# Kernel tuning notes

Hardware: AMD Instinct MI355X
Metric: run time of the kernel (lower is better)

## Reference

```python
import jax, jax.numpy as jnp
import numpy as np

N_NODES = 100000
N_EDGES = 1600000
IN_F, HID_F, N_CLS = 512, 128, 64


def spmm(row, col, val, x, n):
    # out[i] = sum_{e: row[e]==i} val[e] * x[col[e]]  (sparse adj @ x)
    msgs = val[:, None] * x[col]          # [E, F] gather + scale
    return jax.ops.segment_sum(msgs, row, num_segments=n)


def setup_inputs() -> dict:
    key = jax.random.key(0)
    k = jax.random.split(key, 8)
    x = jax.random.normal(k[0], (N_NODES, IN_F), dtype=jnp.float32)
    adj_row = jax.random.randint(k[1], (N_EDGES,), 0, N_NODES, dtype=jnp.int32)
    adj_col = jax.random.randint(k[2], (N_EDGES,), 0, N_NODES, dtype=jnp.int32)
    adj_val = jax.random.uniform(k[3], (N_EDGES,), dtype=jnp.float32)
    s1 = 1.0 / np.sqrt(IN_F)
    s2 = 1.0 / np.sqrt(HID_F)
    w1 = jax.random.uniform(k[4], (IN_F, HID_F), jnp.float32, -s1, s1)
    b1 = jax.random.uniform(k[5], (HID_F,), jnp.float32, -s1, s1)
    w2 = jax.random.uniform(k[6], (HID_F, N_CLS), jnp.float32, -s2, s2)
    b2 = jax.random.uniform(k[7], (N_CLS,), jnp.float32, -s2, s2)
    return {"x": x, "adj_row": adj_row, "adj_col": adj_col, "adj_val": adj_val,
            "w1": w1, "b1": b1, "w2": w2, "b2": b2}


def reference(x, adj_row, adj_col, adj_val, w1, b1, w2, b2):
    n = x.shape[0]
    # conv1: dense projection then sparse aggregation
    h = spmm(adj_row, adj_col, adj_val, x @ w1 + b1, n)
    h = jax.nn.relu(h)  # dropout is identity in eval mode
    # conv2
    out = spmm(adj_row, adj_col, adj_val, h @ w2 + b2, n)
    return out
```

## Files before the change

kernel.cpp:

```cpp
#include <hip/hip_runtime.h>
#include <hip/hip_bf16.h>


constexpr int N_NODES = 100000;
constexpr int IN_F    = 512;
constexpr int HID_F   = 128;
constexpr int N_CLS   = 64;
constexpr int N_EDGES = 1600000;

constexpr int SCAN_BLOCK    = 256;
constexpr int N_SCAN_BLOCKS = (N_NODES + SCAN_BLOCK - 1) / SCAN_BLOCK;
constexpr int NB_GEMM2      = (N_NODES + 255) / 256;

constexpr int NB_G1 = (N_NODES + 63) / 64;
constexpr int NB_SC = (N_EDGES + 1023) / 1024;
constexpr int NB_FUSED = NB_G1 + NB_SC;

typedef __attribute__((ext_vector_type(8))) short short8;
typedef __attribute__((ext_vector_type(4))) float f32x4;

static __device__ __forceinline__ unsigned short f2bf(float x) {
    unsigned int u = __float_as_uint(x);
    unsigned int r = (u + 0x7FFFu + ((u >> 16) & 1u)) >> 16;
    return (unsigned short)r;
}
static __device__ __forceinline__ float bf2f(unsigned short u) {
    return __uint_as_float(((unsigned int)u) << 16);
}

__global__ __launch_bounds__(256) void prep_kernel(
    const float* __restrict__ w1, const float* __restrict__ w2,
    const int* __restrict__ row,
    unsigned short* __restrict__ w1t, unsigned short* __restrict__ w2t,
    int* __restrict__ counts)
{
    const int bid = blockIdx.x;
    if (bid < 256) {
        int idx = bid * 256 + threadIdx.x;
        int n = idx >> 9, k = idx & 511;
        w1t[idx] = f2bf(w1[k * HID_F + n]);
    } else if (bid < 288) {
        int idx = (bid - 256) * 256 + threadIdx.x;
        int n = idx >> 7, k = idx & 127;
        w2t[idx] = f2bf(w2[k * N_CLS + n]);
    } else {
        int e = (bid - 288) * 256 + threadIdx.x;
        if (e < N_EDGES) atomicAdd(&counts[row[e]], 1);
    }
}

__global__ __launch_bounds__(SCAN_BLOCK) void scanA_kernel(
    const int* __restrict__ counts, int* __restrict__ local_ex,
    int* __restrict__ blockSums)
{
    __shared__ int s[SCAN_BLOCK];
    const int t = threadIdx.x;
    const int i = blockIdx.x * SCAN_BLOCK + t;
    int v = (i < N_NODES) ? counts[i] : 0;
    s[t] = v;
    __syncthreads();
    for (int off = 1; off < SCAN_BLOCK; off <<= 1) {
        int u = (t >= off) ? s[t - off] : 0;
        __syncthreads();
        s[t] += u;
        __syncthreads();
    }
    if (i < N_NODES) local_ex[i] = s[t] - v;
    if (t == SCAN_BLOCK - 1) blockSums[blockIdx.x] = s[t];
}

__global__ __launch_bounds__(512) void scanB_kernel(int* __restrict__ blockSums)
{
    __shared__ int s[512];
    const int t = threadIdx.x;
    int v = (t < N_SCAN_BLOCKS) ? blockSums[t] : 0;
    s[t] = v;
    __syncthreads();
    for (int off = 1; off < 512; off <<= 1) {
        int u = (t >= off) ? s[t - off] : 0;
        __syncthreads();
        s[t] += u;
        __syncthreads();
    }
    if (t < N_SCAN_BLOCKS) blockSums[t] = s[t] - v;
}

__global__ __launch_bounds__(SCAN_BLOCK) void scanC_kernel(
    const int* __restrict__ local_ex, const int* __restrict__ blockSums,
    int* __restrict__ row_ptr, int* __restrict__ cursor)
{
    const int i = blockIdx.x * SCAN_BLOCK + threadIdx.x;
    if (i < N_NODES) {
        int v = local_ex[i] + blockSums[blockIdx.x];
        row_ptr[i] = v;
        cursor[i]  = v;
    }
    if (i == 0) row_ptr[N_NODES] = N_EDGES;
}

__global__ __launch_bounds__(256, 4) void fused_g1_scatter_kernel(
    const float* __restrict__ x, const unsigned short* __restrict__ w1t,
    const float* __restrict__ b1, unsigned short* __restrict__ h0b,
    const int* __restrict__ row, const int* __restrict__ col,
    const float* __restrict__ val, int* __restrict__ cursor,
    int2* __restrict__ es)
{
    __shared__ unsigned short Bs[128 * 128];
    char* lb = (char*)Bs;
    const int tid = threadIdx.x;
    const int bid = blockIdx.x;

    if (bid & 1) {
        const int base = (bid >> 1) * 1024 + tid;
#pragma unroll
        for (int i = 0; i < 4; ++i) {
            int e = base + i * 256;
            if (e < N_EDGES) {
                int r = row[e];
                int pos = atomicAdd(&cursor[r], 1);
                es[pos] = make_int2(col[e], __float_as_int(val[e]));
            }
        }
        return;
    }

    const int gid  = bid >> 1;
    const int lane = tid & 63;
    const int w    = tid >> 6;
    const int m = lane & 15;
    const int q = lane >> 4;
    const int row0 = gid * 64;
    const int myrow = row0 + w * 16 + m;
    const int arow  = (myrow < N_NODES) ? myrow : (N_NODES - 1);

    f32x4 acc[8];
#pragma unroll
    for (int ni = 0; ni < 8; ++ni)
        acc[ni] = (f32x4){0.f, 0.f, 0.f, 0.f};

    union U8 { short8 v; __hip_bfloat162 h[4]; };

    const float* ap = x + (size_t)arow * IN_F + q * 8;
    const int swz = (m & 7) << 4;

    float4 a0l = ((const float4*)ap)[0];
    float4 a0h = ((const float4*)ap)[1];
    float4 a1l = ((const float4*)(ap + 32))[0];
    float4 a1h = ((const float4*)(ap + 32))[1];

#pragma unroll
    for (int t = 0; t < 16; ++t) {
        if ((t & 3) == 0) {
            if (t) __syncthreads();
            const unsigned short* src = w1t + (t >> 2) * 128;
#pragma unroll
            for (int i = 0; i < 8; ++i) {
                int c = tid + i * 256;
                int n = c >> 4, k16 = c & 15;
                short8 v = *(const short8*)(src + (size_t)n * IN_F + k16 * 8);
                *(short8*)(lb + ((n * 256 + k16 * 16) ^ ((n & 7) << 4))) = v;
            }
            __syncthreads();
        }

        float4 nl, nh;
        if (t + 2 < 16) {
            nl = ((const float4*)(ap + (t + 2) * 32))[0];
            nh = ((const float4*)(ap + (t + 2) * 32))[1];
        }

        U8 u;
        u.h[0] = __float22bfloat162_rn(make_float2(a0l.x, a0l.y));
        u.h[1] = __float22bfloat162_rn(make_float2(a0l.z, a0l.w));
        u.h[2] = __float22bfloat162_rn(make_float2(a0h.x, a0h.y));
        u.h[3] = __float22bfloat162_rn(make_float2(a0h.z, a0h.w));
        short8 av = u.v;

        const int kb = (t & 3) * 64 + q * 16;
#pragma unroll
        for (int ni = 0; ni < 8; ++ni) {
            int off = (((ni * 16 + m) << 8) + kb) ^ swz;
            short8 bfr = *(const short8*)(lb + off);
            acc[ni] = __builtin_amdgcn_mfma_f32_16x16x32_bf16(av, bfr, acc[ni], 0, 0, 0);
        }

        a0l = a1l; a0h = a1h; a1l = nl; a1h = nh;
    }

    __syncthreads();
    {
        float bias[8];
#pragma unroll
        for (int ni = 0; ni < 8; ++ni) bias[ni] = b1[ni * 16 + m];

        char* cb = lb + w * 4352;
#pragma unroll
        for (int ni = 0; ni < 8; ++ni)
#pragma unroll
            for (int r = 0; r < 4; ++r)
                *(unsigned short*)(cb + (q * 4 + r) * 272 + (ni * 16 + m) * 2) =
                    f2bf(acc[ni][r] + bias[ni]);
    }
    __syncthreads();
#pragma unroll
    for (int i = 0; i < 4; ++i) {
        int c = tid + i * 256;
        int lr = c >> 4, c16 = c & 15;
        int grow = row0 + lr;
        if (grow < N_NODES) {
            short8 v = *(const short8*)(lb + (lr >> 4) * 4352 + (lr & 15) * 272 + c16 * 16);
            *(short8*)(h0b + (size_t)grow * HID_F + c16 * 8) = v;
        }
    }
}

__global__ __launch_bounds__(512, 4) void gemm2_mfma_kernel(
    const unsigned short* __restrict__ h1r, const unsigned short* __restrict__ w2t,
    const float* __restrict__ b2, float* __restrict__ h2)
{
    __shared__ unsigned short Bs[64 * 128];
    char* lb = (char*)Bs;

    const int tid  = threadIdx.x;
    const int lane = tid & 63;
    const int w    = tid >> 6;
    const int m = lane & 15;
    const int q = lane >> 4;
    const int row0 = blockIdx.x * 256 + w * 32;
    const bool active = row0 < N_NODES;

#pragma unroll
    for (int i = 0; i < 2; ++i) {
        int chunk = tid + i * 512;
        int n   = chunk >> 4;
        int k16 = chunk & 15;
        short8 v = *(const short8*)(w2t + (size_t)n * HID_F + k16 * 8);
        *(short8*)(lb + ((n * 256 + k16 * 16) ^ ((n & 7) << 4))) = v;
    }
    __syncthreads();
    if (!active) return;

    const unsigned short* a0p = h1r + (size_t)(row0 + m)      * HID_F + q * 8;
    const unsigned short* a1p = h1r + (size_t)(row0 + 16 + m) * HID_F + q * 8;

    short8 a0[4], a1[4];
#pragma unroll
    for (int t = 0; t < 4; ++t) {
        a0[t] = *(const short8*)(a0p + t * 32);
        a1[t] = *(const short8*)(a1p + t * 32);
    }

    f32x4 acc[2][4];
#pragma unroll
    for (int mi = 0; mi < 2; ++mi)
#pragma unroll
        for (int ni = 0; ni < 4; ++ni)
            acc[mi][ni] = (f32x4){0.f, 0.f, 0.f, 0.f};

    const int swz = (m & 7) << 4;
#pragma unroll
    for (int t = 0; t < 4; ++t) {
        const int kb = t * 64 + q * 16;
#pragma unroll
        for (int ni = 0; ni < 4; ++ni) {
            int off = (((ni * 16 + m) << 8) + kb) ^ swz;
            short8 b = *(const short8*)(lb + off);
            acc[0][ni] = __builtin_amdgcn_mfma_f32_16x16x32_bf16(a0[t], b, acc[0][ni], 0, 0, 0);
            acc[1][ni] = __builtin_amdgcn_mfma_f32_16x16x32_bf16(a1[t], b, acc[1][ni], 0, 0, 0);
        }
    }

    float bias[4];
#pragma unroll
    for (int ni = 0; ni < 4; ++ni) bias[ni] = b2[ni * 16 + m];

#pragma unroll
    for (int mi = 0; mi < 2; ++mi)
#pragma unroll
        for (int r = 0; r < 4; ++r) {
            int row = row0 + mi * 16 + q * 4 + r;
            float* dst = h2 + (size_t)row * N_CLS;
#pragma unroll
            for (int ni = 0; ni < 4; ++ni)
                dst[ni * 16 + m] = acc[mi][ni][r] + bias[ni];
        }
}

__global__ __launch_bounds__(256) void spmm_g128_kernel(
    const int* __restrict__ rp, const int2* __restrict__ es,
    const unsigned short* __restrict__ src, unsigned short* __restrict__ dst)
{
    const int r = blockIdx.x * 4 + threadIdx.y;
    if (r >= N_NODES) return;
    const int lane = threadIdx.x;
    const int j0 = rp[r], j1 = rp[r + 1];

    float ax = 0.f, ay = 0.f;
    int j = j0;
    for (; j + 7 < j1; j += 8) {
        int2 e[8];
        ushort2 u[8];
#pragma unroll
        for (int t = 0; t < 8; ++t) e[t] = es[j + t];
#pragma unroll
        for (int t = 0; t < 8; ++t)
            u[t] = ((const ushort2*)(src + (size_t)e[t].x * HID_F))[lane];
#pragma unroll
        for (int t = 0; t < 8; ++t) {
            float v = __int_as_float(e[t].y);
            ax += v * bf2f(u[t].x);
            ay += v * bf2f(u[t].y);
        }
    }
    if (j + 3 < j1) {
        int2 e[4];
        ushort2 u[4];
#pragma unroll
        for (int t = 0; t < 4; ++t) e[t] = es[j + t];
#pragma unroll
        for (int t = 0; t < 4; ++t)
            u[t] = ((const ushort2*)(src + (size_t)e[t].x * HID_F))[lane];
#pragma unroll
        for (int t = 0; t < 4; ++t) {
            float v = __int_as_float(e[t].y);
            ax += v * bf2f(u[t].x);
            ay += v * bf2f(u[t].y);
        }
        j += 4;
    }
    for (; j < j1; ++j) {
        int2 e = es[j];
        float v = __int_as_float(e.y);
        ushort2 u = ((const ushort2*)(src + (size_t)e.x * HID_F))[lane];
        ax += v * bf2f(u.x);
        ay += v * bf2f(u.y);
    }
    ushort2 o;
    o.x = f2bf(fmaxf(ax, 0.f));
    o.y = f2bf(fmaxf(ay, 0.f));
    ((ushort2*)(dst + (size_t)r * HID_F))[lane] = o;
}

__global__ __launch_bounds__(256) void spmm_g64_kernel(
    const int* __restrict__ rp, const int2* __restrict__ es,
    const float* __restrict__ src, float* __restrict__ dst)
{
    const int r = blockIdx.x * 4 + threadIdx.y;
    if (r >= N_NODES) return;
    const int lane = threadIdx.x;
    const int j0 = rp[r], j1 = rp[r + 1];

    float acc = 0.f;
    int j = j0;
    for (; j + 7 < j1; j += 8) {
        int2 e[8];
        float a[8];
#pragma unroll
        for (int t = 0; t < 8; ++t) e[t] = es[j + t];
#pragma unroll
        for (int t = 0; t < 8; ++t)
            a[t] = src[(size_t)e[t].x * N_CLS + lane];
#pragma unroll
        for (int t = 0; t < 8; ++t)
            acc += __int_as_float(e[t].y) * a[t];
    }
    if (j + 3 < j1) {
        int2 e[4];
        float a[4];
#pragma unroll
        for (int t = 0; t < 4; ++t) e[t] = es[j + t];
#pragma unroll
        for (int t = 0; t < 4; ++t)
            a[t] = src[(size_t)e[t].x * N_CLS + lane];
#pragma unroll
        for (int t = 0; t < 4; ++t)
            acc += __int_as_float(e[t].y) * a[t];
        j += 4;
    }
    for (; j < j1; ++j) {
        int2 e = es[j];
        acc += __int_as_float(e.y) * src[(size_t)e.x * N_CLS + lane];
    }
    dst[(size_t)r * N_CLS + lane] = acc;
}

extern "C" void kernel_launch(void* const* d_in, const int* in_sizes, int n_in,
                              void* d_out, int out_size, void* d_ws, size_t ws_size,
                              hipStream_t stream)
{
    const float* x       = (const float*)d_in[0];
    const int*   adj_row = (const int*)  d_in[1];
    const int*   adj_col = (const int*)  d_in[2];
    const float* adj_val = (const float*)d_in[3];
    const float* w1      = (const float*)d_in[4];
    const float* b1      = (const float*)d_in[5];
    const float* w2      = (const float*)d_in[6];
    const float* b2      = (const float*)d_in[7];
    float*       out     = (float*)d_out;

    char* ws = (char*)d_ws;
    unsigned short* h0b   = (unsigned short*)ws;
    unsigned short* h1r   = (unsigned short*)(ws + 25600000);
    float*          h2    = (float*)(ws + 51200000);
    int2*           es    = (int2*) (ws + 76800000);
    int*            rp    = (int*)  (ws + 89600000);
    int*            cur   = (int*)  (ws + 90000016);
    unsigned short* w1t   = (unsigned short*)(ws + 90400016);
    int*            lex   = (int*)  (ws + 90531088);
    int*            bsum  = (int*)  (ws + 90931088);
    unsigned short* w2t   = (unsigned short*)(ws + 90932656);

    hipMemsetAsync(cur, 0, N_NODES * sizeof(int), stream);
    prep_kernel<<<288 + (N_EDGES + 255) / 256, 256, 0, stream>>>(
        w1, w2, adj_row, w1t, w2t, cur);
    scanA_kernel<<<N_SCAN_BLOCKS, SCAN_BLOCK, 0, stream>>>(cur, lex, bsum);
    scanB_kernel<<<1, 512, 0, stream>>>(bsum);
    scanC_kernel<<<N_SCAN_BLOCKS, SCAN_BLOCK, 0, stream>>>(lex, bsum, rp, cur);

    fused_g1_scatter_kernel<<<NB_FUSED, 256, 0, stream>>>(
        x, w1t, b1, h0b, adj_row, adj_col, adj_val, cur, es);
    spmm_g128_kernel<<<(N_NODES + 3) / 4, dim3(64, 4), 0, stream>>>(
        rp, es, h0b, h1r);

    gemm2_mfma_kernel<<<NB_GEMM2, 512, 0, stream>>>(h1r, w2t, b2, h2);
    spmm_g64_kernel<<<(N_NODES + 3) / 4, dim3(64, 4), 0, stream>>>(
        rp, es, h2, out);
}
```

Measured before the change: 563.2 us.

## Fuse first SpMM into GEMM2 via LDS and gather 4 edges per wave

Measured after the change: 659.5 us. 1.17x slower.

```diff
diff --git a/kernel.cpp b/kernel.cpp
--- a/kernel.cpp
+++ b/kernel.cpp
@@ -10,11 +10,11 @@
 
 constexpr int SCAN_BLOCK    = 256;
 constexpr int N_SCAN_BLOCKS = (N_NODES + SCAN_BLOCK - 1) / SCAN_BLOCK;
-constexpr int NB_GEMM2      = (N_NODES + 255) / 256;
 
 constexpr int NB_G1 = (N_NODES + 63) / 64;
 constexpr int NB_SC = (N_EDGES + 1023) / 1024;
 constexpr int NB_FUSED = NB_G1 + NB_SC;
+constexpr int NB_S1G2  = (N_NODES + 127) / 128;
 
 typedef __attribute__((ext_vector_type(8))) short short8;
 typedef __attribute__((ext_vector_type(4))) float f32x4;
@@ -214,59 +214,106 @@
     }
 }
 
-__global__ __launch_bounds__(512, 4) void gemm2_mfma_kernel(
-    const unsigned short* __restrict__ h1r, const unsigned short* __restrict__ w2t,
-    const float* __restrict__ b2, float* __restrict__ h2)
-{
-    __shared__ unsigned short Bs[64 * 128];
-    char* lb = (char*)Bs;
+__global__ __launch_bounds__(256, 3) void spmm1_gemm2_kernel(
+    const int* __restrict__ rp, const int2* __restrict__ es,
+    const unsigned short* __restrict__ h0b,
+    const unsigned short* __restrict__ w2t, const float* __restrict__ b2,
+    float* __restrict__ h2)
+{
+    __shared__ unsigned short H1[128 * 128];
+    __shared__ unsigned short W2[64 * 128];
+    char* lh = (char*)H1;
+    char* lw = (char*)W2;
 
     const int tid  = threadIdx.x;
     const int lane = tid & 63;
     const int w    = tid >> 6;
+    const int g    = lane >> 4;
+    const int l    = lane & 15;
+    const int row0 = blockIdx.x * 128;
+
+#pragma unroll
+    for (int i = 0; i < 4; ++i) {
+        int chunk = tid + i * 256;
+        int n = chunk >> 4, k16 = chunk & 15;
+        short8 v = *(const short8*)(w2t + (size_t)n * HID_F + k16 * 8);
+        *(short8*)(lw + ((n * 256 + k16 * 16) ^ ((n & 7) << 4))) = v;
+    }
+
+    for (int rr = 0; rr < 32; ++rr) {
+        const int r = row0 + w * 32 + rr;
+        if (r < N_NODES) {
+            const int j0 = rp[r], j1 = rp[r + 1];
+            float acc[8] = {0.f, 0.f, 0.f, 0.f, 0.f, 0.f, 0.f, 0.f};
+            int j = j0;
+            if (j < j1) {
+                int jj = j + g;
+                int ci = jj < j1 ? jj : j1 - 1;
+                int2 ec = es[ci];
+                float vc = jj < j1 ? __int_as_float(ec.y) : 0.f;
+                for (; j < j1; j += 4) {
+                    int2 en = ec; float vn = 0.f;
+                    if (j + 4 < j1) {
+                        int jn = j + 4 + g;
+                        int cn = jn < j1 ? jn : j1 - 1;
+                        en = es[cn];
+                        vn = jn < j1 ? __int_as_float(en.y) : 0.f;
+                    }
+                    if (vc != 0.f) {
+                        union { short8 v; unsigned short u[8]; } hv;
+                        hv.v = *(const short8*)(h0b + (size_t)ec.x * HID_F + l * 8);
+#pragma unroll
+                        for (int t = 0; t < 8; ++t)
+                            acc[t] += vc * bf2f(hv.u[t]);
+                    }
+                    ec = en; vc = vn;
+                }
+            }
+#pragma unroll
+            for (int t = 0; t < 8; ++t) {
+                acc[t] += __shfl_xor(acc[t], 16, 64);
+                acc[t] += __shfl_xor(acc[t], 32, 64);
+            }
+            if (g == 0) {
+                union { short8 v; __hip_bfloat162 h[4]; } o;
+                o.h[0] = __float22bfloat162_rn(make_float2(fmaxf(acc[0], 0.f), fmaxf(acc[1], 0.f)));
+                o.h[1] = __float22bfloat162_rn(make_float2(fmaxf(acc[2], 0.f), fmaxf(acc[3], 0.f)));
+                o.h[2] = __float22bfloat162_rn(make_float2(fmaxf(acc[4], 0.f), fmaxf(acc[5], 0.f)));
+                o.h[3] = __float22bfloat162_rn(make_float2(fmaxf(acc[6], 0.f), fmaxf(acc[7], 0.f)));
+                const int lr = w * 32 + rr;
+                *(short8*)(lh + ((lr * 256 + l * 16) ^ ((lr & 7) << 4))) = o.v;
+            }
+        }
+    }
+    __syncthreads();
+
     const int m = lane & 15;
     const int q = lane >> 4;
-    const int row0 = blockIdx.x * 256 + w * 32;
-    const bool active = row0 < N_NODES;
-
-#pragma unroll
-    for (int i = 0; i < 2; ++i) {
-        int chunk = tid + i * 512;
-        int n   = chunk >> 4;
-        int k16 = chunk & 15;
-        short8 v = *(const short8*)(w2t + (size_t)n * HID_F + k16 * 8);
-        *(short8*)(lb + ((n * 256 + k16 * 16) ^ ((n & 7) << 4))) = v;
-    }
-    __syncthreads();
-    if (!active) return;
-
-    const unsigned short* a0p = h1r + (size_t)(row0 + m)      * HID_F + q * 8;
-    const unsigned short* a1p = h1r + (size_t)(row0 + 16 + m) * HID_F + q * 8;
+    const int r0l = w * 32 + m;
+    const int r1l = w * 32 + 16 + m;
 
     short8 a0[4], a1[4];
 #pragma unroll
     for (int t = 0; t < 4; ++t) {
-        a0[t] = *(const short8*)(a0p + t * 32);
-        a1[t] = *(const short8*)(a1p + t * 32);
-    }
-
-    f32x4 acc[2][4];
+        a0[t] = *(const short8*)(lh + ((r0l * 256 + t * 64 + q * 16) ^ ((r0l & 7) << 4)));
+        a1[t] = *(const short8*)(lh + ((r1l * 256 + t * 64 + q * 16) ^ ((r1l & 7) << 4)));
+    }
+
+    f32x4 acc2[2][4];
 #pragma unroll
     for (int mi = 0; mi < 2; ++mi)
 #pragma unroll
         for (int ni = 0; ni < 4; ++ni)
-            acc[mi][ni] = (f32x4){0.f, 0.f, 0.f, 0.f};
-
-    const int swz = (m & 7) << 4;
+            acc2[mi][ni] = (f32x4){0.f, 0.f, 0.f, 0.f};
+
 #pragma unroll
     for (int t = 0; t < 4; ++t) {
         const int kb = t * 64 + q * 16;
 #pragma unroll
         for (int ni = 0; ni < 4; ++ni) {
-            int off = (((ni * 16 + m) << 8) + kb) ^ swz;
-            short8 b = *(const short8*)(lb + off);
-            acc[0][ni] = __builtin_amdgcn_mfma_f32_16x16x32_bf16(a0[t], b, acc[0][ni], 0, 0, 0);
-            acc[1][ni] = __builtin_amdgcn_mfma_f32_16x16x32_bf16(a1[t], b, acc[1][ni], 0, 0, 0);
+            short8 b = *(const short8*)(lw + ((((ni * 16 + m) << 8) + kb) ^ ((m & 7) << 4)));
+            acc2[0][ni] = __builtin_amdgcn_mfma_f32_16x16x32_bf16(a0[t], b, acc2[0][ni], 0, 0, 0);
+            acc2[1][ni] = __builtin_amdgcn_mfma_f32_16x16x32_bf16(a1[t], b, acc2[1][ni], 0, 0, 0);
         }
     }
 
@@ -277,111 +324,61 @@
 #pragma unroll
     for (int mi = 0; mi < 2; ++mi)
 #pragma unroll
-        for (int r = 0; r < 4; ++r) {
-            int row = row0 + mi * 16 + q * 4 + r;
-            float* dst = h2 + (size_t)row * N_CLS;
-#pragma unroll
-            for (int ni = 0; ni < 4; ++ni)
-                dst[ni * 16 + m] = acc[mi][ni][r] + bias[ni];
-        }
-}
-
-__global__ __launch_bounds__(256) void spmm_g128_kernel(
+        for (int rt = 0; rt < 4; ++rt) {
+            int grow = row0 + w * 32 + mi * 16 + q * 4 + rt;
+            if (grow < N_NODES) {
+                float* dst = h2 + (size_t)grow * N_CLS;
+#pragma unroll
+                for (int ni = 0; ni < 4; ++ni)
+                    dst[ni * 16 + m] = acc2[mi][ni][rt] + bias[ni];
+            }
+        }
+}
+
+__global__ __launch_bounds__(256) void spmm2_kernel(
     const int* __restrict__ rp, const int2* __restrict__ es,
-    const unsigned short* __restrict__ src, unsigned short* __restrict__ dst)
+    const float* __restrict__ src, float* __restrict__ dst)
 {
     const int r = blockIdx.x * 4 + threadIdx.y;
     if (r >= N_NODES) return;
     const int lane = threadIdx.x;
+    const int g = lane >> 4;
+    const int l = lane & 15;
     const int j0 = rp[r], j1 = rp[r + 1];
 
-    float ax = 0.f, ay = 0.f;
+    float acc[4] = {0.f, 0.f, 0.f, 0.f};
     int j = j0;
-    for (; j + 7 < j1; j += 8) {
-        int2 e[8];
-        ushort2 u[8];
-#pragma unroll
-        for (int t = 0; t < 8; ++t) e[t] = es[j + t];
-#pragma unroll
-        for (int t = 0; t < 8; ++t)
-            u[t] = ((const ushort2*)(src + (size_t)e[t].x * HID_F))[lane];
-#pragma unroll
-        for (int t = 0; t < 8; ++t) {
-            float v = __int_as_float(e[t].y);
-            ax += v * bf2f(u[t].x);
-            ay += v * bf2f(u[t].y);
-        }
-    }
-    if (j + 3 < j1) {
-        int2 e[4];
-        ushort2 u[4];
-#pragma unroll
-        for (int t = 0; t < 4; ++t) e[t] = es[j + t];
-#pragma unroll
-        for (int t = 0; t < 4; ++t)
-            u[t] = ((const ushort2*)(src + (size_t)e[t].x * HID_F))[lane];
-#pragma unroll
-        for (int t = 0; t < 4; ++t) {
-            float v = __int_as_float(e[t].y);
-            ax += v * bf2f(u[t].x);
-            ay += v * bf2f(u[t].y);
-        }
-        j += 4;
-    }
-    for (; j < j1; ++j) {
-        int2 e = es[j];
-        float v = __int_as_float(e.y);
-        ushort2 u = ((const ushort2*)(src + (size_t)e.x * HID_F))[lane];
-        ax += v * bf2f(u.x);
-        ay += v * bf2f(u.y);
-    }
-    ushort2 o;
-    o.x = f2bf(fmaxf(ax, 0.f));
-    o.y = f2bf(fmaxf(ay, 0.f));
-    ((ushort2*)(dst + (size_t)r * HID_F))[lane] = o;
-}
-
-__global__ __launch_bounds__(256) void spmm_g64_kernel(
-    const int* __restrict__ rp, const int2* __restrict__ es,
-    const float* __restrict__ src, float* __restrict__ dst)
-{
-    const int r = blockIdx.x * 4 + threadIdx.y;
-    if (r >= N_NODES) return;
-    const int lane = threadIdx.x;
-    const int j0 = rp[r], j1 = rp[r + 1];
-
-    float acc = 0.f;
-    int j = j0;
-    for (; j + 7 < j1; j += 8) {
-        int2 e[8];
-        float a[8];
-#pragma unroll
-        for (int t = 0; t < 8; ++t) e[t] = es[j + t];
-#pragma unroll
-        for (int t = 0; t < 8; ++t)
-            a[t] = src[(size_t)e[t].x * N_CLS + lane];
-#pragma unroll
-        for (int t = 0; t < 8; ++t)
-            acc += __int_as_float(e[t].y) * a[t];
-    }
-    if (j + 3 < j1) {
-        int2 e[4];
-        float a[4];
-#pragma unroll
-        for (int t = 0; t < 4; ++t) e[t] = es[j + t];
-#pragma unroll
-        for (int t = 0; t < 4; ++t)
-            a[t] = src[(size_t)e[t].x * N_CLS + lane];
-#pragma unroll
-        for (int t = 0; t < 4; ++t)
-            acc += __int_as_float(e[t].y) * a[t];
-        j += 4;
-    }
-    for (; j < j1; ++j) {
-        int2 e = es[j];
-        acc += __int_as_float(e.y) * src[(size_t)e.x * N_CLS + lane];
-    }
-    dst[(size_t)r * N_CLS + lane] = acc;
+    if (j < j1) {
+        int jj = j + g;
+        int ci = jj < j1 ? jj : j1 - 1;
+        int2 ec = es[ci];
+        float vc = jj < j1 ? __int_as_float(ec.y) : 0.f;
+        for (; j < j1; j += 4) {
+            int2 en = ec; float vn = 0.f;
+            if (j + 4 < j1) {
+                int jn = j + 4 + g;
+                int cn = jn < j1 ? jn : j1 - 1;
+                en = es[cn];
+                vn = jn < j1 ? __int_as_float(en.y) : 0.f;
+            }
+            if (vc != 0.f) {
+                float4 hv = *(const float4*)(src + (size_t)ec.x * N_CLS + l * 4);
+                acc[0] += vc * hv.x;
+                acc[1] += vc * hv.y;
+                acc[2] += vc * hv.z;
+                acc[3] += vc * hv.w;
+            }
+            ec = en; vc = vn;
+        }
+    }
+#pragma unroll
+    for (int t = 0; t < 4; ++t) {
+        acc[t] += __shfl_xor(acc[t], 16, 64);
+        acc[t] += __shfl_xor(acc[t], 32, 64);
+    }
+    if (g == 0)
+        *(float4*)(dst + (size_t)r * N_CLS + l * 4) =
+            make_float4(acc[0], acc[1], acc[2], acc[3]);
 }
 
 extern "C" void kernel_launch(void* const* d_in, const int* in_sizes, int n_in,
@@ -400,7 +397,6 @@
 
     char* ws = (char*)d_ws;
     unsigned short* h0b   = (unsigned short*)ws;
-    unsigned short* h1r   = (unsigned short*)(ws + 25600000);
     float*          h2    = (float*)(ws + 51200000);
     int2*           es    = (int2*) (ws + 76800000);
     int*            rp    = (int*)  (ws + 89600000);
@@ -419,10 +415,9 @@
 
     fused_g1_scatter_kernel<<<NB_FUSED, 256, 0, stream>>>(
         x, w1t, b1, h0b, adj_row, adj_col, adj_val, cur, es);
-    spmm_g128_kernel<<<(N_NODES + 3) / 4, dim3(64, 4), 0, stream>>>(
-        rp, es, h0b, h1r);
-
-    gemm2_mfma_kernel<<<NB_GEMM2, 512, 0, stream>>>(h1r, w2t, b2, h2);
-    spmm_g64_kernel<<<(N_NODES + 3) / 4, dim3(64, 4), 0, stream>>>(
+
+    spmm1_gemm2_kernel<<<NB_S1G2, 256, 0, stream>>>(rp, es, h0b, w2t, b2, h2);
+
+    spmm2_kernel<<<(N_NODES + 3) / 4, dim3(64, 4), 0, stream>>>(
         rp, es, h2, out);
 }
```
